# Kernel tuning notes

Hardware: AMD Instinct MI355X
Metric: run time of the kernel (lower is better)

## Reference

```python
import jax, jax.numpy as jnp
import numpy as np

KERNEL = 5
PADDING = 2
STRIDE = 2
MIXTURES = 2
OUT_CH = 128


def setup_inputs() -> dict:
    key = jax.random.key(0)
    ks = jax.random.split(key, 7)
    B, CIN, H, W = 8, 64, 128, 128
    return {
        "x": jax.random.normal(ks[0], (B, CIN, H, W), jnp.float32),
        "w_q": jax.random.normal(ks[1], (OUT_CH, CIN), jnp.float32) * 0.05,
        "w_k": jax.random.normal(ks[2], (OUT_CH, CIN), jnp.float32) * 0.05,
        "w_v": jax.random.normal(ks[3], (OUT_CH * MIXTURES, CIN), jnp.float32) * 0.05,
        "row_emb": jax.random.normal(ks[4], (OUT_CH, KERNEL), jnp.float32),
        "col_emb": jax.random.normal(ks[5], (OUT_CH, KERNEL), jnp.float32),
        "mix_emb": jax.random.normal(ks[6], (OUT_CH, MIXTURES), jnp.float32),
    }


def _patches(t, stride):
    # im2col, matching torch nn.Unfold channel-major ordering: [B, C*k*k, Ho, Wo]
    return jax.lax.conv_general_dilated_patches(
        t, (KERNEL, KERNEL), (stride, stride),
        padding=[(PADDING, PADDING), (PADDING, PADDING)])


def reference(x, w_q, w_k, w_v, row_emb, col_emb, mix_emb):
    K2 = KERNEL * KERNEL
    # 1x1 convolutions (groups=1, no bias)
    q = jnp.einsum('bchw,oc->bohw', x, w_q)            # [B,C,H,W]
    k = jnp.einsum('bchw,oc->bohw', x, w_k)            # [B,C,H,W]
    v = jnp.einsum('bchw,oc->bohw', x, w_v)            # [B,C*M,H,W]

    # key patches: [B, C, K2, Ho, Wo]
    kp = _patches(k, STRIDE)
    B, _, Ho, Wo = kp.shape
    kp = kp.reshape(B, OUT_CH, K2, Ho, Wo)

    # queries at strided output locations (unfold with kernel 1, stride s)
    qs = q[:, :, ::STRIDE, ::STRIDE]                   # [B,C,Ho,Wo]

    # attention over the local window, softmax along K2
    scores = jnp.einsum('bchw,bckhw->bkhw', qs, kp)    # [B,K2,Ho,Wo]
    attn = jax.nn.softmax(scores, axis=1)

    # mixture positional weights: sum_c (row[c,i]+col[c,j]) * mix[c,m] -> [M,k,k]
    wpos = (jnp.einsum('ci,cm->mi', row_emb, mix_emb)[:, :, None]
            + jnp.einsum('cj,cm->mj', col_emb, mix_emb)[:, None, :])
    wpos = jax.nn.softmax(wpos, axis=0).reshape(MIXTURES, K2)  # softmax over mixtures

    # value patches: [B, C, M, K2, Ho, Wo] (channel-major as in torch reshape)
    vp = _patches(v, STRIDE).reshape(B, OUT_CH, MIXTURES, K2, Ho, Wo)
    vals = jnp.einsum('bcmkhw,mk->bckhw', vp, wpos)    # mixture-weighted values

    # attention-weighted sum over the window
    out = jnp.einsum('bckhw,bkhw->bchw', vals, attn)   # [B,C,Ho,Wo]
    return out
```

## Files before the change

### kernel.cpp

```cpp
#include <hip/hip_runtime.h>

typedef unsigned int   uint_;
typedef unsigned short u16;
typedef _Float16 f16;
typedef __attribute__((ext_vector_type(8))) _Float16 f16x8;
typedef __attribute__((ext_vector_type(2))) __fp16 h2;
typedef __attribute__((ext_vector_type(4))) float f4;

#define B_    8
#define CIN_  64
#define H_    128
#define W_    128
#define OC_   128
#define HO_   64
#define WO_   64
#define NPOS  (B_ * HO_ * WO_)

#define XBT_OFF  0
#define MF_OFF   4194304
#define WF_OFF   4196352
#define WPOS_OFF 4204544

__device__ __forceinline__ u16 f2h_bits(float x) {
  return __builtin_bit_cast(u16, (f16)x);
}
__device__ __forceinline__ uint_ cvt_pk_u(float lo, float hi) {
  return __builtin_bit_cast(uint_, __builtin_amdgcn_cvt_pkrtz(lo, hi));
}
template <int N>
__device__ __forceinline__ float ror_add(float x) {
  float r;
  if constexpr (N == 1)
    asm("v_add_f32 %0, %1, %1 row_ror:1" : "=v"(r) : "v"(x));
  else if constexpr (N == 2)
    asm("v_add_f32 %0, %1, %1 row_ror:2" : "=v"(r) : "v"(x));
  else if constexpr (N == 4)
    asm("v_add_f32 %0, %1, %1 row_ror:4" : "=v"(r) : "v"(x));
  else
    asm("v_add_f32 %0, %1, %1 row_ror:8" : "=v"(r) : "v"(x));
  return r;
}
__device__ __forceinline__ void mix_lo(float& acc, uint_ a, uint_ b) {
  asm("v_fma_mix_f32 %0, %1, %2, %0 op_sel:[0,0,0] op_sel_hi:[1,1,0]"
      : "+v"(acc) : "v"(a), "v"(b));
}
__device__ __forceinline__ void mix_hi(float& acc, uint_ a, uint_ b) {
  asm("v_fma_mix_f32 %0, %1, %2, %0 op_sel:[1,1,0] op_sel_hi:[1,1,0]"
      : "+v"(acc) : "v"(a), "v"(b));
}
__device__ __forceinline__ void pk_fma(uint_& acc, uint_ x, uint_ c) {
  asm("v_pk_fma_f16 %0, %1, %2, %0" : "+v"(acc) : "v"(x), "v"(c));
}
__device__ __forceinline__ uint_ pk_mul(uint_ a, uint_ b) {
  uint_ r;
  asm("v_pk_mul_f16 %0, %1, %2" : "=v"(r) : "v"(a), "v"(b));
  return r;
}

__global__ __launch_bounds__(256) void mega_kernel(
    const float* __restrict__ x, u16* __restrict__ xbt,
    const float* __restrict__ w_q, const float* __restrict__ w_k,
    const float* __restrict__ w_v,
    const float* __restrict__ row_emb, const float* __restrict__ col_emb,
    const float* __restrict__ mix_emb,
    u16* __restrict__ MF, u16* __restrict__ WF, uint_* __restrict__ wpk) {
  if (blockIdx.x < 1024) {
    __shared__ float tile[64][129];
    int by = blockIdx.x;
    int b = by >> 7, y = by & 127;
    const float* xp = x + (size_t)b * (CIN_ * H_ * W_) + (size_t)y * W_;
    #pragma unroll
    for (int it = 0; it < 32; ++it) {
      int idx = threadIdx.x + it * 256;
      int c = idx >> 7, xw = idx & 127;
      tile[c][xw] = xp[(size_t)c * (H_ * W_) + xw];
    }
    __syncthreads();
    uint_* dst = (uint_*)(xbt + ((size_t)(b * H_ + y)) * (W_ * 64));
    #pragma unroll
    for (int it = 0; it < 16; ++it) {
      int idx = threadIdx.x + it * 256;
      int xw = idx >> 5, cp = idx & 31;
      dst[idx] = cvt_pk_u(tile[2 * cp][xw], tile[2 * cp + 1][xw]);
    }
  } else {
    int pb = blockIdx.x - 1024;
    if (pb < 16) {
      int idx = pb * 256 + threadIdx.x;
      int a = idx >> 6, c = idx & 63;
      float acc = 0.f;
      #pragma unroll 8
      for (int o = 0; o < 128; ++o)
        acc = fmaf(w_q[o * 64 + a], w_k[o * 64 + c], acc);
      int m = c >> 4, lr = c & 15;
      int ks = a >> 5, q = (a >> 3) & 3, jr = a & 7;
      int off = ((ks * 4 + m) * 64 + (lr + 16 * q)) * 8 + jr;
      MF[off] = f2h_bits(acc * 1.44269504f);
    } else if (pb == 16) {
      int p = threadIdx.x;
      if (p < 25) {
        int i = p / 5, j = p % 5;
        float a0 = 0.f, a1 = 0.f;
        for (int c = 0; c < 128; ++c) {
          float rc = row_emb[c * 5 + i] + col_emb[c * 5 + j];
          a0 = fmaf(rc, mix_emb[c * 2 + 0], a0);
          a1 = fmaf(rc, mix_emb[c * 2 + 1], a1);
        }
        float mx = fmaxf(a0, a1);
        float e0 = __expf(a0 - mx), e1 = __expf(a1 - mx);
        float inv = 1.f / (e0 + e1);
        wpk[p]      = cvt_pk_u(e0 * inv, e0 * inv);
        wpk[32 + p] = cvt_pk_u(e1 * inv, e1 * inv);
      }
    } else {
      int t = (pb - 17) * 256 + threadIdx.x;
      #pragma unroll
      for (int e = 0; e < 4; ++e) {
        int elem = t * 4 + e;
        int c = elem >> 7, k = elem & 127;
        int m = c >> 4, lr = c & 15;
        int ks = k >> 5, q = (k >> 3) & 3, j = k & 7;
        int off = ((ks * 8 + m) * 64 + (lr + 16 * q)) * 8 + j;
        WF[off] = f2h_bits(w_v[elem]);
      }
    }
  }
}

__global__ __launch_bounds__(512) void attn_out_kernel(
    const u16* __restrict__ xbt, const u16* __restrict__ MF,
    const uint_* __restrict__ wpk, const u16* __restrict__ WF,
    float* __restrict__ out) {
  __shared__ u16 Xl[5 * 67 * 64];
  __shared__ union {
    float Ul[32][68];
    u16   Gl[32][136];
  } GU;

  int tid = threadIdx.x;
  int wave = tid >> 6, lane = tid & 63;
  int lr = lane & 15, q = lane >> 4;

  int bid = (int)blockIdx.x;
  int swz = (bid & 7) * 128 + (bid >> 3);
  int pos0 = swz * 32;

  int b = pos0 >> 12;
  int ho0 = (pos0 >> 6) & 63;
  int y0 = 2 * ho0, x0base = 2 * (pos0 & 63);

  {
    int sl = tid & 15;
    int pi0 = tid >> 4;
    const u16* xbb = xbt + (size_t)b * (H_ * W_ * 64);
    #pragma unroll
    for (int it = 0; it < 11; ++it) {
      int pi = it * 32 + pi0;
      if (pi < 335) {
        int row = pi / 67;
        int col = pi - row * 67;
        int yr = y0 + row - 2, xr = x0base + col - 2;
        bool oob = ((unsigned)yr >= (unsigned)H_) | ((unsigned)xr >= (unsigned)W_);
        int yc = min(max(yr, 0), H_ - 1);
        int xc = min(max(xr, 0), W_ - 1);
        uint2 d = *(const uint2*)(xbb + ((size_t)yc * W_ + xc) * 64 + sl * 4);
        if (oob) { d.x = 0u; d.y = 0u; }
        *(uint2*)(&Xl[pi * 64 + sl * 4]) = d;
      }
    }
  }

  {
    int pt = wave >> 2, mm = wave & 3;
    int pu = pos0 + pt * 16 + lr;
    int bu = pu >> 12, hou = (pu >> 6) & 63, wou = pu & 63;
    const u16* xq = xbt + ((size_t)(bu * H_ + 2 * hou) * W_ + 2 * wou) * 64;
    f4 ua = (f4)0.f;
    #pragma unroll
    for (int ks = 0; ks < 2; ++ks) {
      f16x8 bb = *reinterpret_cast<const f16x8*>(xq + ks * 32 + q * 8);
      f16x8 ah = *reinterpret_cast<const f16x8*>(
          MF + ((ks * 4 + mm) * 64 + lane) * 8);
      ua = __builtin_amdgcn_mfma_f32_16x16x32_f16(ah, bb, ua, 0, 0, 0);
    }
    #pragma unroll
    for (int r = 0; r < 4; ++r)
      GU.Ul[pt * 16 + lr][mm * 16 + q * 4 + r] = ua[r];
  }
  __syncthreads();

  {
    int r = wave * 4 + q;
    const u16* xl0 = &Xl[(2 * r) * 64 + lr * 4];

    f4 u = *reinterpret_cast<const f4*>(&GU.Ul[r][lr * 4]);
    uint_ u01 = cvt_pk_u(u.x, u.y);
    uint_ u23 = cvt_pk_u(u.z, u.w);

    float Z0 = 0.f, Z1 = 0.f;
    uint_ g0a = 0u, g0b = 0u, g1a = 0u, g1b = 0u;

    #pragma unroll
    for (int p = 0; p < 25; ++p) {
      const int dy = p / 5, dx = p % 5;
      uint2 d = *(const uint2*)(xl0 + (dy * 67 + dx) * 64);
      float sp = -0.5f;
      mix_lo(sp, d.x, u01);
      mix_hi(sp, d.x, u01);
      mix_lo(sp, d.y, u23);
      mix_hi(sp, d.y, u23);
      sp = ror_add<1>(sp);
      sp = ror_add<2>(sp);
      sp = ror_add<4>(sp);
      sp = ror_add<8>(sp);
      float e = __builtin_amdgcn_exp2f(sp);
      if (p & 1) Z1 += e; else Z0 += e;
      uint_ epk = cvt_pk_u(e, e);
      uint_ c0 = pk_mul(epk, wpk[p]);
      uint_ c1 = pk_mul(epk, wpk[32 + p]);
      pk_fma(g0a, d.x, c0);
      pk_fma(g0b, d.y, c0);
      pk_fma(g1a, d.x, c1);
      pk_fma(g1b, d.y, c1);
    }
    float rZ = 1.f / (Z0 + Z1);
    uint_ rZpk = cvt_pk_u(rZ, rZ);

    uint2 w0, w1;
    w0.x = pk_mul(g0a, rZpk); w0.y = pk_mul(g0b, rZpk);
    w1.x = pk_mul(g1a, rZpk); w1.y = pk_mul(g1b, rZpk);
    *(uint2*)&GU.Gl[r][lr * 4] = w0;
    *(uint2*)&GU.Gl[r][64 + lr * 4] = w1;
  }

  __syncthreads();

  {
    f4 acc0 = (f4)0.f, acc1 = (f4)0.f;
    #pragma unroll
    for (int ks = 0; ks < 4; ++ks) {
      f16x8 b0 = *reinterpret_cast<const f16x8*>(&GU.Gl[lr][ks * 32 + q * 8]);
      f16x8 b1 = *reinterpret_cast<const f16x8*>(&GU.Gl[16 + lr][ks * 32 + q * 8]);
      f16x8 ah = *reinterpret_cast<const f16x8*>(
          WF + ((ks * 8 + wave) * 64 + lane) * 8);
      acc0 = __builtin_amdgcn_mfma_f32_16x16x32_f16(ah, b0, acc0, 0, 0, 0);
      acc1 = __builtin_amdgcn_mfma_f32_16x16x32_f16(ah, b1, acc1, 0, 0, 0);
    }
    int bb = pos0 >> 12;
    int hw0 = pos0 & 4095;
    float* op = out + (size_t)bb * (OC_ * HO_ * WO_) + hw0;
    #pragma unroll
    for (int rr = 0; rr < 4; ++rr) {
      int c = wave * 16 + q * 4 + rr;
      op[(size_t)c * 4096 + lr] = acc0[rr];
      op[(size_t)c * 4096 + 16 + lr] = acc1[rr];
    }
  }
}

extern "C" void kernel_launch(void* const* d_in, const int* in_sizes, int n_in,
                              void* d_out, int out_size, void* d_ws, size_t ws_size,
                              hipStream_t stream) {
  const float* x       = (const float*)d_in[0];
  const float* w_q     = (const float*)d_in[1];
  const float* w_k     = (const float*)d_in[2];
  const float* w_v     = (const float*)d_in[3];
  const float* row_emb = (const float*)d_in[4];
  const float* col_emb = (const float*)d_in[5];
  const float* mix_emb = (const float*)d_in[6];
  float* out = (float*)d_out;

  float* ws   = (float*)d_ws;
  u16*   xbt  = (u16*)(ws + XBT_OFF);
  u16*   MF   = (u16*)(ws + MF_OFF);
  u16*   WF   = (u16*)(ws + WF_OFF);
  uint_* wpk  = (uint_*)(ws + WPOS_OFF);

  mega_kernel<<<1024 + 33, 256, 0, stream>>>(x, xbt, w_q, w_k, w_v, row_emb,
                                             col_emb, mix_emb, MF, WF, wpk);
  attn_out_kernel<<<NPOS / 32, 512, 0, stream>>>(xbt, MF, wpk, WF, out);
}
```

Baseline: 35.40 us.

## Fuse NCHW-to-NHWC fp16 transpose into attention kernel, drop xbt intermediate

Removes the separate transpose pass that wrote an fp16 channels-last copy of x to global memory. Each attention block now loads its 5x67 window straight from the fp32 NCHW input, transposes it through a shared-memory staging tile, and packs it to fp16 in LDS. The query input is then read from that LDS tile instead of global memory. This saves the intermediate write and re-read, at the cost of extra barriers, redundant reloads of halo rows across neighbouring blocks, and a larger shared-memory union that may lower occupancy.

```diff
diff --git a/kernel.cpp b/kernel.cpp
--- a/kernel.cpp
+++ b/kernel.cpp
@@ -16,7 +16,6 @@
 #define WO_   64
 #define NPOS  (B_ * HO_ * WO_)
 
-#define XBT_OFF  0
 #define MF_OFF   4194304
 #define WF_OFF   4196352
 #define WPOS_OFF 4204544
@@ -57,85 +56,64 @@
   return r;
 }
 
-__global__ __launch_bounds__(256) void mega_kernel(
-    const float* __restrict__ x, u16* __restrict__ xbt,
+__global__ __launch_bounds__(256) void prep_kernel(
     const float* __restrict__ w_q, const float* __restrict__ w_k,
     const float* __restrict__ w_v,
     const float* __restrict__ row_emb, const float* __restrict__ col_emb,
     const float* __restrict__ mix_emb,
     u16* __restrict__ MF, u16* __restrict__ WF, uint_* __restrict__ wpk) {
-  if (blockIdx.x < 1024) {
-    __shared__ float tile[64][129];
-    int by = blockIdx.x;
-    int b = by >> 7, y = by & 127;
-    const float* xp = x + (size_t)b * (CIN_ * H_ * W_) + (size_t)y * W_;
-    #pragma unroll
-    for (int it = 0; it < 32; ++it) {
-      int idx = threadIdx.x + it * 256;
-      int c = idx >> 7, xw = idx & 127;
-      tile[c][xw] = xp[(size_t)c * (H_ * W_) + xw];
-    }
-    __syncthreads();
-    uint_* dst = (uint_*)(xbt + ((size_t)(b * H_ + y)) * (W_ * 64));
-    #pragma unroll
-    for (int it = 0; it < 16; ++it) {
-      int idx = threadIdx.x + it * 256;
-      int xw = idx >> 5, cp = idx & 31;
-      dst[idx] = cvt_pk_u(tile[2 * cp][xw], tile[2 * cp + 1][xw]);
+  int pb = blockIdx.x;
+  if (pb < 16) {
+    int idx = pb * 256 + threadIdx.x;
+    int a = idx >> 6, c = idx & 63;
+    float acc = 0.f;
+    #pragma unroll 8
+    for (int o = 0; o < 128; ++o)
+      acc = fmaf(w_q[o * 64 + a], w_k[o * 64 + c], acc);
+    int m = c >> 4, lr = c & 15;
+    int ks = a >> 5, q = (a >> 3) & 3, jr = a & 7;
+    int off = ((ks * 4 + m) * 64 + (lr + 16 * q)) * 8 + jr;
+    MF[off] = f2h_bits(acc * 1.44269504f);
+  } else if (pb == 16) {
+    int p = threadIdx.x;
+    if (p < 25) {
+      int i = p / 5, j = p % 5;
+      float a0 = 0.f, a1 = 0.f;
+      for (int c = 0; c < 128; ++c) {
+        float rc = row_emb[c * 5 + i] + col_emb[c * 5 + j];
+        a0 = fmaf(rc, mix_emb[c * 2 + 0], a0);
+        a1 = fmaf(rc, mix_emb[c * 2 + 1], a1);
+      }
+      float mx = fmaxf(a0, a1);
+      float e0 = __expf(a0 - mx), e1 = __expf(a1 - mx);
+      float inv = 1.f / (e0 + e1);
+      wpk[p]      = cvt_pk_u(e0 * inv, e0 * inv);
+      wpk[32 + p] = cvt_pk_u(e1 * inv, e1 * inv);
     }
   } else {
-    int pb = blockIdx.x - 1024;
-    if (pb < 16) {
-      int idx = pb * 256 + threadIdx.x;
-      int a = idx >> 6, c = idx & 63;
-      float acc = 0.f;
-      #pragma unroll 8
-      for (int o = 0; o < 128; ++o)
-        acc = fmaf(w_q[o * 64 + a], w_k[o * 64 + c], acc);
+    int t = (pb - 17) * 256 + threadIdx.x;
+    #pragma unroll
+    for (int e = 0; e < 4; ++e) {
+      int elem = t * 4 + e;
+      int c = elem >> 7, k = elem & 127;
       int m = c >> 4, lr = c & 15;
-      int ks = a >> 5, q = (a >> 3) & 3, jr = a & 7;
-      int off = ((ks * 4 + m) * 64 + (lr + 16 * q)) * 8 + jr;
-      MF[off] = f2h_bits(acc * 1.44269504f);
-    } else if (pb == 16) {
-      int p = threadIdx.x;
-      if (p < 25) {
-        int i = p / 5, j = p % 5;
-        float a0 = 0.f, a1 = 0.f;
-        for (int c = 0; c < 128; ++c) {
-          float rc = row_emb[c * 5 + i] + col_emb[c * 5 + j];
-          a0 = fmaf(rc, mix_emb[c * 2 + 0], a0);
-          a1 = fmaf(rc, mix_emb[c * 2 + 1], a1);
-        }
-        float mx = fmaxf(a0, a1);
-        float e0 = __expf(a0 - mx), e1 = __expf(a1 - mx);
-        float inv = 1.f / (e0 + e1);
-        wpk[p]      = cvt_pk_u(e0 * inv, e0 * inv);
-        wpk[32 + p] = cvt_pk_u(e1 * inv, e1 * inv);
-      }
-    } else {
-      int t = (pb - 17) * 256 + threadIdx.x;
-      #pragma unroll
-      for (int e = 0; e < 4; ++e) {
-        int elem = t * 4 + e;
-        int c = elem >> 7, k = elem & 127;
-        int m = c >> 4, lr = c & 15;
-        int ks = k >> 5, q = (k >> 3) & 3, j = k & 7;
-        int off = ((ks * 8 + m) * 64 + (lr + 16 * q)) * 8 + j;
-        WF[off] = f2h_bits(w_v[elem]);
-      }
+      int ks = k >> 5, q = (k >> 3) & 3, j = k & 7;
+      int off = ((ks * 8 + m) * 64 + (lr + 16 * q)) * 8 + j;
+      WF[off] = f2h_bits(w_v[elem]);
     }
   }
 }
 
 __global__ __launch_bounds__(512) void attn_out_kernel(
-    const u16* __restrict__ xbt, const u16* __restrict__ MF,
+    const float* __restrict__ x, const u16* __restrict__ MF,
     const uint_* __restrict__ wpk, const u16* __restrict__ WF,
     float* __restrict__ out) {
   __shared__ u16 Xl[5 * 67 * 64];
   __shared__ union {
+    float tmp[64][68];
     float Ul[32][68];
     u16   Gl[32][136];
-  } GU;
+  } S;
 
   int tid = threadIdx.x;
   int wave = tid >> 6, lane = tid & 63;
@@ -150,31 +128,46 @@
   int y0 = 2 * ho0, x0base = 2 * (pos0 & 63);
 
   {
-    int sl = tid & 15;
-    int pi0 = tid >> 4;
-    const u16* xbb = xbt + (size_t)b * (H_ * W_ * 64);
-    #pragma unroll
-    for (int it = 0; it < 11; ++it) {
-      int pi = it * 32 + pi0;
-      if (pi < 335) {
-        int row = pi / 67;
-        int col = pi - row * 67;
-        int yr = y0 + row - 2, xr = x0base + col - 2;
-        bool oob = ((unsigned)yr >= (unsigned)H_) | ((unsigned)xr >= (unsigned)W_);
-        int yc = min(max(yr, 0), H_ - 1);
-        int xc = min(max(xr, 0), W_ - 1);
-        uint2 d = *(const uint2*)(xbb + ((size_t)yc * W_ + xc) * 64 + sl * 4);
-        if (oob) { d.x = 0u; d.y = 0u; }
-        *(uint2*)(&Xl[pi * 64 + sl * 4]) = d;
+    const float* xb = x + (size_t)b * (CIN_ * H_ * W_);
+    int sE = tid & 7;
+    int cE = tid >> 3;
+    int slc = tid & 31;
+    int cb = tid >> 5;
+    #pragma unroll 1
+    for (int r = 0; r < 5; ++r) {
+      int y = y0 + r - 2;
+      bool oy = ((unsigned)y >= (unsigned)H_);
+      int yc = min(max(y, 0), H_ - 1);
+      const float* xrow = xb + ((size_t)cE * H_ + yc) * W_;
+      #pragma unroll
+      for (int k = 0; k < 5; ++k) {
+        int s = sE + k * 8;
+        if (s < 34) {
+          int xc = x0base - 2 + 2 * s;
+          int xcc = min(max(xc, 0), W_ - 2);
+          float2 d = *(const float2*)(xrow + xcc);
+          float v0 = (oy || (unsigned)xc >= (unsigned)W_) ? 0.f : d.x;
+          float v1 = (oy || (unsigned)(xc + 1) >= (unsigned)W_) ? 0.f : d.y;
+          *(float2*)&S.tmp[cE][2 * s] = make_float2(v0, v1);
+        }
       }
+      __syncthreads();
+      #pragma unroll
+      for (int k = 0; k < 5; ++k) {
+        int col = cb + k * 16;
+        if (col < 67) {
+          uint_ pk = cvt_pk_u(S.tmp[2 * slc][col], S.tmp[2 * slc + 1][col]);
+          *(uint_*)&Xl[(r * 67 + col) * 64 + 2 * slc] = pk;
+        }
+      }
+      __syncthreads();
     }
   }
 
   {
     int pt = wave >> 2, mm = wave & 3;
-    int pu = pos0 + pt * 16 + lr;
-    int bu = pu >> 12, hou = (pu >> 6) & 63, wou = pu & 63;
-    const u16* xq = xbt + ((size_t)(bu * H_ + 2 * hou) * W_ + 2 * wou) * 64;
+    int rloc = pt * 16 + lr;
+    const u16* xq = &Xl[(2 * 67 + 2 + 2 * rloc) * 64];
     f4 ua = (f4)0.f;
     #pragma unroll
     for (int ks = 0; ks < 2; ++ks) {
@@ -183,9 +176,10 @@
           MF + ((ks * 4 + mm) * 64 + lane) * 8);
       ua = __builtin_amdgcn_mfma_f32_16x16x32_f16(ah, bb, ua, 0, 0, 0);
     }
+    __syncthreads();
     #pragma unroll
     for (int r = 0; r < 4; ++r)
-      GU.Ul[pt * 16 + lr][mm * 16 + q * 4 + r] = ua[r];
+      S.Ul[pt * 16 + lr][mm * 16 + q * 4 + r] = ua[r];
   }
   __syncthreads();
 
@@ -193,7 +187,7 @@
     int r = wave * 4 + q;
     const u16* xl0 = &Xl[(2 * r) * 64 + lr * 4];
 
-    f4 u = *reinterpret_cast<const f4*>(&GU.Ul[r][lr * 4]);
+    f4 u = *reinterpret_cast<const f4*>(&S.Ul[r][lr * 4]);
     uint_ u01 = cvt_pk_u(u.x, u.y);
     uint_ u23 = cvt_pk_u(u.z, u.w);
 
@@ -229,8 +223,8 @@
     uint2 w0, w1;
     w0.x = pk_mul(g0a, rZpk); w0.y = pk_mul(g0b, rZpk);
     w1.x = pk_mul(g1a, rZpk); w1.y = pk_mul(g1b, rZpk);
-    *(uint2*)&GU.Gl[r][lr * 4] = w0;
-    *(uint2*)&GU.Gl[r][64 + lr * 4] = w1;
+    *(uint2*)&S.Gl[r][lr * 4] = w0;
+    *(uint2*)&S.Gl[r][64 + lr * 4] = w1;
   }
 
   __syncthreads();
@@ -239,8 +233,8 @@
     f4 acc0 = (f4)0.f, acc1 = (f4)0.f;
     #pragma unroll
     for (int ks = 0; ks < 4; ++ks) {
-      f16x8 b0 = *reinterpret_cast<const f16x8*>(&GU.Gl[lr][ks * 32 + q * 8]);
-      f16x8 b1 = *reinterpret_cast<const f16x8*>(&GU.Gl[16 + lr][ks * 32 + q * 8]);
+      f16x8 b0 = *reinterpret_cast<const f16x8*>(&S.Gl[lr][ks * 32 + q * 8]);
+      f16x8 b1 = *reinterpret_cast<const f16x8*>(&S.Gl[16 + lr][ks * 32 + q * 8]);
       f16x8 ah = *reinterpret_cast<const f16x8*>(
           WF + ((ks * 8 + wave) * 64 + lane) * 8);
       acc0 = __builtin_amdgcn_mfma_f32_16x16x32_f16(ah, b0, acc0, 0, 0, 0);
@@ -271,12 +265,11 @@
   float* out = (float*)d_out;
 
   float* ws   = (float*)d_ws;
-  u16*   xbt  = (u16*)(ws + XBT_OFF);
   u16*   MF   = (u16*)(ws + MF_OFF);
   u16*   WF   = (u16*)(ws + WF_OFF);
   uint_* wpk  = (uint_*)(ws + WPOS_OFF);
 
-  mega_kernel<<<1024 + 33, 256, 0, stream>>>(x, xbt, w_q, w_k, w_v, row_emb,
-                                             col_emb, mix_emb, MF, WF, wpk);
-  attn_out_kernel<<<NPOS / 32, 512, 0, stream>>>(xbt, MF, wpk, WF, out);
-}
+  prep_kernel<<<33, 256, 0, stream>>>(w_q, w_k, w_v, row_emb, col_emb,
+                                      mix_emb, MF, WF, wpk);
+  attn_out_kernel<<<NPOS / 32, 512, 0, stream>>>(x, MF, wpk, WF, out);
+}
```

After: 44.81 us. 1.27x slower.

## Halve attention tile to 16 positions per block and vectorize transpose loads

Applied to the files above, without the earlier changes.

The attention kernel now handles 16 output positions per 256-thread block instead of 32 per 512-thread block. This shrinks the LDS halo tile and the score/gather buffers and sets a launch-bounds occupancy hint, so more blocks can be resident per CU. Each wave now runs two output MFMA groups in sequence. The cost is a larger halo overlap fraction, which means more redundant global loads of the input patch. The mega kernel's x-transpose also switches to float4 global reads and uint2 writes.

```diff
diff --git a/kernel.cpp b/kernel.cpp
--- a/kernel.cpp
+++ b/kernel.cpp
@@ -70,18 +70,26 @@
     int b = by >> 7, y = by & 127;
     const float* xp = x + (size_t)b * (CIN_ * H_ * W_) + (size_t)y * W_;
     #pragma unroll
-    for (int it = 0; it < 32; ++it) {
-      int idx = threadIdx.x + it * 256;
-      int c = idx >> 7, xw = idx & 127;
-      tile[c][xw] = xp[(size_t)c * (H_ * W_) + xw];
+    for (int it = 0; it < 8; ++it) {
+      int idx2 = threadIdx.x + it * 256;
+      int c = idx2 >> 5, xq4 = idx2 & 31;
+      float4 v = *reinterpret_cast<const float4*>(
+          xp + (size_t)c * (H_ * W_) + 4 * xq4);
+      tile[c][4 * xq4 + 0] = v.x;
+      tile[c][4 * xq4 + 1] = v.y;
+      tile[c][4 * xq4 + 2] = v.z;
+      tile[c][4 * xq4 + 3] = v.w;
     }
     __syncthreads();
-    uint_* dst = (uint_*)(xbt + ((size_t)(b * H_ + y)) * (W_ * 64));
-    #pragma unroll
-    for (int it = 0; it < 16; ++it) {
-      int idx = threadIdx.x + it * 256;
-      int xw = idx >> 5, cp = idx & 31;
-      dst[idx] = cvt_pk_u(tile[2 * cp][xw], tile[2 * cp + 1][xw]);
+    uint2* dst2 = (uint2*)(xbt + ((size_t)(b * H_ + y)) * (W_ * 64));
+    #pragma unroll
+    for (int it = 0; it < 8; ++it) {
+      int idx2 = threadIdx.x + it * 256;
+      int xw = idx2 >> 4, cp2 = idx2 & 15;
+      uint2 w;
+      w.x = cvt_pk_u(tile[4 * cp2 + 0][xw], tile[4 * cp2 + 1][xw]);
+      w.y = cvt_pk_u(tile[4 * cp2 + 2][xw], tile[4 * cp2 + 3][xw]);
+      dst2[xw * 16 + cp2] = w;
     }
   } else {
     int pb = blockIdx.x - 1024;
@@ -127,14 +135,14 @@
   }
 }
 
-__global__ __launch_bounds__(512) void attn_out_kernel(
+__global__ __launch_bounds__(256, 6) void attn_out_kernel(
     const u16* __restrict__ xbt, const u16* __restrict__ MF,
     const uint_* __restrict__ wpk, const u16* __restrict__ WF,
     float* __restrict__ out) {
-  __shared__ u16 Xl[5 * 67 * 64];
+  __shared__ u16 Xl[5 * 35 * 64];
   __shared__ union {
-    float Ul[32][68];
-    u16   Gl[32][136];
+    float Ul[16][68];
+    u16   Gl[16][136];
   } GU;
 
   int tid = threadIdx.x;
@@ -142,8 +150,8 @@
   int lr = lane & 15, q = lane >> 4;
 
   int bid = (int)blockIdx.x;
-  int swz = (bid & 7) * 128 + (bid >> 3);
-  int pos0 = swz * 32;
+  int swz = (bid & 7) * 256 + (bid >> 3);
+  int pos0 = swz * 16;
 
   int b = pos0 >> 12;
   int ho0 = (pos0 >> 6) & 63;
@@ -155,10 +163,10 @@
     const u16* xbb = xbt + (size_t)b * (H_ * W_ * 64);
     #pragma unroll
     for (int it = 0; it < 11; ++it) {
-      int pi = it * 32 + pi0;
-      if (pi < 335) {
-        int row = pi / 67;
-        int col = pi - row * 67;
+      int pi = it * 16 + pi0;
+      if (pi < 175) {
+        int row = pi / 35;
+        int col = pi - row * 35;
         int yr = y0 + row - 2, xr = x0base + col - 2;
         bool oob = ((unsigned)yr >= (unsigned)H_) | ((unsigned)xr >= (unsigned)W_);
         int yc = min(max(yr, 0), H_ - 1);
@@ -171,8 +179,8 @@
   }
 
   {
-    int pt = wave >> 2, mm = wave & 3;
-    int pu = pos0 + pt * 16 + lr;
+    int mm = wave;
+    int pu = pos0 + lr;
     int bu = pu >> 12, hou = (pu >> 6) & 63, wou = pu & 63;
     const u16* xq = xbt + ((size_t)(bu * H_ + 2 * hou) * W_ + 2 * wou) * 64;
     f4 ua = (f4)0.f;
@@ -185,7 +193,7 @@
     }
     #pragma unroll
     for (int r = 0; r < 4; ++r)
-      GU.Ul[pt * 16 + lr][mm * 16 + q * 4 + r] = ua[r];
+      GU.Ul[lr][mm * 16 + q * 4 + r] = ua[r];
   }
   __syncthreads();
 
@@ -203,7 +211,7 @@
     #pragma unroll
     for (int p = 0; p < 25; ++p) {
       const int dy = p / 5, dx = p % 5;
-      uint2 d = *(const uint2*)(xl0 + (dy * 67 + dx) * 64);
+      uint2 d = *(const uint2*)(xl0 + (dy * 35 + dx) * 64);
       float sp = -0.5f;
       mix_lo(sp, d.x, u01);
       mix_hi(sp, d.x, u01);
@@ -236,24 +244,25 @@
   __syncthreads();
 
   {
-    f4 acc0 = (f4)0.f, acc1 = (f4)0.f;
-    #pragma unroll
-    for (int ks = 0; ks < 4; ++ks) {
-      f16x8 b0 = *reinterpret_cast<const f16x8*>(&GU.Gl[lr][ks * 32 + q * 8]);
-      f16x8 b1 = *reinterpret_cast<const f16x8*>(&GU.Gl[16 + lr][ks * 32 + q * 8]);
-      f16x8 ah = *reinterpret_cast<const f16x8*>(
-          WF + ((ks * 8 + wave) * 64 + lane) * 8);
-      acc0 = __builtin_amdgcn_mfma_f32_16x16x32_f16(ah, b0, acc0, 0, 0, 0);
-      acc1 = __builtin_amdgcn_mfma_f32_16x16x32_f16(ah, b1, acc1, 0, 0, 0);
-    }
     int bb = pos0 >> 12;
     int hw0 = pos0 & 4095;
     float* op = out + (size_t)bb * (OC_ * HO_ * WO_) + hw0;
     #pragma unroll
-    for (int rr = 0; rr < 4; ++rr) {
-      int c = wave * 16 + q * 4 + rr;
-      op[(size_t)c * 4096 + lr] = acc0[rr];
-      op[(size_t)c * 4096 + 16 + lr] = acc1[rr];
+    for (int t = 0; t < 2; ++t) {
+      int mm = wave + t * 4;
+      f4 acc = (f4)0.f;
+      #pragma unroll
+      for (int ks = 0; ks < 4; ++ks) {
+        f16x8 b0 = *reinterpret_cast<const f16x8*>(&GU.Gl[lr][ks * 32 + q * 8]);
+        f16x8 ah = *reinterpret_cast<const f16x8*>(
+            WF + ((ks * 8 + mm) * 64 + lane) * 8);
+        acc = __builtin_amdgcn_mfma_f32_16x16x32_f16(ah, b0, acc, 0, 0, 0);
+      }
+      #pragma unroll
+      for (int rr = 0; rr < 4; ++rr) {
+        int c = mm * 16 + q * 4 + rr;
+        op[(size_t)c * 4096 + lr] = acc[rr];
+      }
     }
   }
 }
@@ -278,5 +287,5 @@
 
   mega_kernel<<<1024 + 33, 256, 0, stream>>>(x, xbt, w_q, w_k, w_v, row_emb,
                                              col_emb, mix_emb, MF, WF, wpk);
-  attn_out_kernel<<<NPOS / 32, 512, 0, stream>>>(xbt, MF, wpk, WF, out);
-}
+  attn_out_kernel<<<NPOS / 16, 256, 0, stream>>>(xbt, MF, wpk, WF, out);
+}
```

Result: no change. 35.25 us (-0.4%).
